# Kernel optimization log

Hardware: AMD Instinct MI355X
Metric: run time of the kernel (lower is better)

Reference implementation:

```python
import jax, jax.numpy as jnp
import numpy as np

B, T = 128, 512
V, P, K = 10002, 500, 20
DC, DP, DT = 300, 100, 50
D = DC + DP + DT
H = 256


def setup_inputs() -> dict:
    key = jax.random.key(0)
    ks = jax.random.split(key, 21)
    s = lambda i, shape: jax.random.normal(ks[i], shape, jnp.float32) * 0.05
    return dict(
        x=jax.random.randint(ks[0], (B, T), 0, V),
        y=jax.random.randint(ks[1], (B, T), 0, K),
        pre_tags=jax.random.randint(ks[2], (B, T), 0, K),
        pinyin_tags=jax.random.randint(ks[3], (B, T), 0, P),
        mask=jnp.ones((B, T), bool),
        char_emb=s(4, (V, DC)),
        tag_emb=s(5, (K, DT)),
        pinyin_emb=s(6, (P, DP)),
        w_ih_f=s(7, (4 * H, D)), w_hh_f=s(8, (4 * H, H)), b_ih_f=s(9, (4 * H,)), b_hh_f=s(10, (4 * H,)),
        w_ih_b=s(11, (4 * H, D)), w_hh_b=s(12, (4 * H, H)), b_ih_b=s(13, (4 * H,)), b_hh_b=s(14, (4 * H,)),
        w_out=s(15, (K, 2 * H)), b_out=s(16, (K,)),
        start_trans=s(17, (K,)), end_trans=s(18, (K,)), trans=s(19, (K, K)),
    )


def _lstm_dir(xs, w_ih, w_hh, b_ih, b_hh, reverse):
    # xs: [T,B,D]; precompute input projection for all steps (one big GEMM)
    pre = jnp.einsum('tbd,gd->tbg', xs, w_ih) + b_ih + b_hh  # [T,B,4H]
    bsz = xs.shape[1]

    def step(carry, gx):
        h, c = carry
        g = gx + h @ w_hh.T
        i, f, gg, o = jnp.split(g, 4, axis=-1)  # torch gate order i,f,g,o
        c = jax.nn.sigmoid(f) * c + jax.nn.sigmoid(i) * jnp.tanh(gg)
        h = jax.nn.sigmoid(o) * jnp.tanh(c)
        return (h, c), h

    init = (jnp.zeros((bsz, H), xs.dtype), jnp.zeros((bsz, H), xs.dtype))
    _, hs = jax.lax.scan(step, init, pre, reverse=reverse)
    return hs  # [T,B,H]


def _emissions(x, pre_tags, pinyin_tags, char_emb, tag_emb, pinyin_emb,
               w_ih_f, w_hh_f, b_ih_f, b_hh_f, w_ih_b, w_hh_b, b_ih_b, b_hh_b,
               w_out, b_out):
    emb = jnp.concatenate([char_emb[x], pinyin_emb[pinyin_tags], tag_emb[pre_tags]], axis=2)  # [B,T,D]
    xs = emb.transpose(1, 0, 2)  # [T,B,D]
    hf = _lstm_dir(xs, w_ih_f, w_hh_f, b_ih_f, b_hh_f, reverse=False)
    hb = _lstm_dir(xs, w_ih_b, w_hh_b, b_ih_b, b_hh_b, reverse=True)
    h = jnp.concatenate([hf, hb], axis=-1)  # [T,B,2H]
    return jnp.einsum('tbh,kh->tbk', h, w_out) + b_out  # emissions [T,B,K]


def _crf_nll(em, tags, mask, start, trans, end):
    # em [T,B,K] (time-major), torchcrf forward with reduction='sum'
    tg = tags.T  # [T,B]
    mk = mask.T.astype(em.dtype)  # [T,B]
    # gold-path score
    first = start[tg[0]] + jnp.take_along_axis(em[0], tg[0][:, None], 1)[:, 0]

    def num_step(score, inputs):
        e_t, t_prev, t_cur, m = inputs
        s = trans[t_prev, t_cur] + jnp.take_along_axis(e_t, t_cur[:, None], 1)[:, 0]
        return score + s * m, None

    score, _ = jax.lax.scan(num_step, first, (em[1:], tg[:-1], tg[1:], mk[1:]))
    last_idx = (mask.sum(1) - 1).astype(jnp.int32)
    last_tag = jnp.take_along_axis(tags, last_idx[:, None].astype(tags.dtype), 1)[:, 0]
    score = score + end[last_tag]
    # partition function via forward algorithm
    alpha0 = start[None, :] + em[0]  # [B,K]

    def den_step(alpha, inputs):
        e_t, m = inputs
        nxt = jax.nn.logsumexp(alpha[:, :, None] + trans[None, :, :] + e_t[:, None, :], axis=1)
        return jnp.where(m[:, None] > 0, nxt, alpha), None

    alpha, _ = jax.lax.scan(den_step, alpha0, (em[1:], mk[1:]))
    logZ = jax.nn.logsumexp(alpha + end[None, :], axis=1)
    llh = jnp.sum(score - logZ)
    return -llh  # module returns -crf(...)


def reference(x, y, pre_tags, pinyin_tags, mask, char_emb, tag_emb, pinyin_emb,
              w_ih_f, w_hh_f, b_ih_f, b_hh_f, w_ih_b, w_hh_b, b_ih_b, b_hh_b,
              w_out, b_out, start_trans, end_trans, trans):
    em = _emissions(x, pre_tags, pinyin_tags, char_emb, tag_emb, pinyin_emb,
                    w_ih_f, w_hh_f, b_ih_f, b_hh_f, w_ih_b, w_hh_b, b_ih_b, b_hh_b,
                    w_out, b_out)
    return _crf_nll(em, y, mask, start_trans, trans, end_trans)
```

## Files before the change

kernel.cpp:

```cpp
#include <hip/hip_runtime.h>
#include <hip/hip_bf16.h>

typedef __attribute__((ext_vector_type(8))) short short8;
typedef __attribute__((ext_vector_type(4))) float float4v;

#if __has_builtin(__builtin_amdgcn_sdot4)
#define DOT4(a, b, c) __builtin_amdgcn_sdot4((int)(a), (int)(b), (c), false)
#else
__device__ __forceinline__ int dot4_(int a, int b, int c) {
  c += (int)(signed char)(a) * (int)(signed char)(b);
  c += (int)(signed char)(a >> 8) * (int)(signed char)(b >> 8);
  c += (int)(signed char)(a >> 16) * (int)(signed char)(b >> 16);
  c += (a >> 24) * (b >> 24);
  return c;
}
#define DOT4(a, b, c) dot4_((int)(a), (int)(b), (c))
#endif

__device__ __forceinline__ float sigmoidf_(float x) {
  return __fdividef(1.f, 1.f + __expf(-x));
}
__device__ __forceinline__ float tanhf_(float x) {
  float e = __expf(2.f * x);
  return 1.f - __fdividef(2.f, e + 1.f);
}
__device__ __forceinline__ float bflo(unsigned int v) {
  return __uint_as_float(v << 16);
}
__device__ __forceinline__ float bfhi(unsigned int v) {
  return __uint_as_float(v & 0xffff0000u);
}

template <int CTRL>
__device__ __forceinline__ int qadd_i(int v) {
  return v + __builtin_amdgcn_update_dpp(0, v, CTRL, 0xF, 0xF, true);
}
template <int CTRL>
__device__ __forceinline__ float qmax_f(float v) {
  int r = __builtin_amdgcn_update_dpp(0, __float_as_int(v), CTRL, 0xF, 0xF, true);
  return fmaxf(v, __int_as_float(r));
}
#define XOR1 0xB1
#define XOR2 0x4E

__device__ __forceinline__ unsigned int pack4_(float4 v, float inv) {
  int b0 = (int)rintf(v.x * inv), b1 = (int)rintf(v.y * inv);
  int b2 = (int)rintf(v.z * inv), b3 = (int)rintf(v.w * inv);
  return (unsigned int)((b0 & 0xff) | ((b1 & 0xff) << 8) | ((b2 & 0xff) << 16) |
                        ((b3 & 0xff) << 24));
}

__global__ __launch_bounds__(256) void proj_gemm(
    const float* __restrict__ A, int rowsA, int Kdim, int col_off,
    const float* __restrict__ wf, const float* __restrict__ wb,
    const float* __restrict__ bf1, const float* __restrict__ bf2,
    const float* __restrict__ bb1, const float* __restrict__ bb2,
    __hip_bfloat16* __restrict__ out, int add_bias) {
  __shared__ __align__(16) __hip_bfloat16 As[64][40];
  __shared__ __align__(16) __hip_bfloat16 Bs[256][40];
  const int tid = threadIdx.x;
  const int m0 = blockIdx.x * 64, n0 = blockIdx.y * 256;
  const int lane = tid & 63, wave = tid >> 6;
  const int quad = lane >> 4, lm = lane & 15;
  float4v acc[16] = {};
  const int ksteps = (Kdim + 31) >> 5;
  const int r = tid >> 2, c0 = (tid & 3) << 3;
  const int rb = tid >> 4, cb = (tid & 15) * 2;
  for (int ks = 0; ks < ksteps; ++ks) {
    const int k0 = ks << 5;
#pragma unroll
    for (int e = 0; e < 8; ++e) {
      int kk = k0 + c0 + e;
      float av = (m0 + r < rowsA && kk < Kdim) ? A[(m0 + r) * Kdim + kk] : 0.f;
      As[r][c0 + e] = __float2bfloat16(av);
    }
#pragma unroll
    for (int j = 0; j < 16; ++j) {
      int n = n0 + rb + 16 * j;
      const float* __restrict__ wrow =
          (n < 1024) ? (wf + n * 450 + col_off) : (wb + (n - 1024) * 450 + col_off);
      int kk = k0 + cb;
      float b0 = 0.f, b1 = 0.f;
      if (kk < Kdim) {
        float2 v = *(const float2*)(wrow + kk);
        b0 = v.x;
        b1 = v.y;
      }
      Bs[rb + 16 * j][cb] = __float2bfloat16(b0);
      Bs[rb + 16 * j][cb + 1] = __float2bfloat16(b1);
    }
    __syncthreads();
    short8 af = *(const short8*)(&As[wave * 16 + lm][quad * 8]);
#pragma unroll
    for (int t = 0; t < 16; ++t) {
      short8 bf = *(const short8*)(&Bs[t * 16 + lm][quad * 8]);
      acc[t] = __builtin_amdgcn_mfma_f32_16x16x32_bf16(af, bf, acc[t], 0, 0, 0);
    }
    __syncthreads();
  }
#pragma unroll
  for (int t = 0; t < 16; ++t) {
#pragma unroll
    for (int rr = 0; rr < 4; ++rr) {
      int m = m0 + wave * 16 + quad * 4 + rr;
      int col = n0 + t * 16 + lm;
      if (m < rowsA) {
        float v = acc[t][rr];
        if (add_bias)
          v += (col < 1024) ? (bf1[col] + bf2[col]) : (bb1[col - 1024] + bb2[col - 1024]);
        int dir = col >> 10, r2 = col & 1023;
        int gate = r2 >> 8, u = r2 & 255;
        out[m * 2048 + dir * 1024 + u * 4 + gate] = __float2bfloat16(v);
      }
    }
  }
}

__global__ __launch_bounds__(256) void lstm_kernel(
    const float* __restrict__ whh_f, const float* __restrict__ whh_b,
    const int* __restrict__ x, const int* __restrict__ ptags, const int* __restrict__ gtags,
    const char* __restrict__ char_proj, const char* __restrict__ pin_proj,
    const char* __restrict__ tag_proj, __hip_bfloat16* __restrict__ h_out) {
  extern __shared__ __align__(16) char smem[];
  uint4* wlds = (uint4*)smem;
  int4* sidx = (int4*)(smem + 65536);
  signed char* hb = (signed char*)(smem + 73728);

  const int tid = threadIdx.x;
  const int q = tid >> 2, e = tid & 3;
  const int chain = blockIdx.x;
  const int dir = chain >> 7;
  const int b = chain & 127;
  const float* __restrict__ whh = dir ? whh_b : whh_f;

  sidx[tid] = make_int4(x[b * 512 + tid] * 4096, ptags[b * 512 + tid] * 4096,
                        gtags[b * 512 + tid] * 4096, 0);
  sidx[tid + 256] = make_int4(x[b * 512 + tid + 256] * 4096, ptags[b * 512 + tid + 256] * 4096,
                              gtags[b * 512 + tid + 256] * 4096, 0);
  if (tid < 32) ((int4*)hb)[tid] = make_int4(0, 0, 0, 0);

  unsigned int Wreg[12][16];
  float sc4[4];
#pragma unroll
  for (int rr = 0; rr < 16; ++rr) {
    const int unit = 4 * q + (rr >> 2), gate = rr & 3;
    const float* __restrict__ wr = whh + (gate * 256 + unit) * 256 + e * 64;
    float mx = 0.f;
#pragma unroll
    for (int k4 = 0; k4 < 16; ++k4) {
      float4 v = ((const float4*)wr)[k4];
      mx = fmaxf(mx, fmaxf(fmaxf(fabsf(v.x), fabsf(v.y)), fmaxf(fabsf(v.z), fabsf(v.w))));
    }
    mx = qmax_f<XOR1>(mx);
    mx = qmax_f<XOR2>(mx);
    float inv = (mx > 0.f) ? __fdividef(127.f, mx) : 0.f;
    float scv = (mx > 0.f) ? (mx / (127.f * 127.f)) : 0.f;
    if ((rr >> 2) == e) sc4[gate] = scv;
    if (rr < 12) {
#pragma unroll
      for (int k4 = 0; k4 < 16; ++k4) Wreg[rr][k4] = pack4_(((const float4*)wr)[k4], inv);
    } else {
      const int p = rr - 12;
#pragma unroll
      for (int c = 0; c < 4; ++c) {
        uint4 tv;
        tv.x = pack4_(((const float4*)wr)[c * 4 + 0], inv);
        tv.y = pack4_(((const float4*)wr)[c * 4 + 1], inv);
        tv.z = pack4_(((const float4*)wr)[c * 4 + 2], inv);
        tv.w = pack4_(((const float4*)wr)[c * 4 + 3], inv);
        wlds[(p * 4 + c) * 256 + tid] = tv;
      }
    }
  }
  __syncthreads();

  const int myu = tid;
  const int pre_off = dir * 2048 + myu * 8;
  float cst = 0.f;
  const uint4* wbase = wlds + tid;

  int t_cur = dir ? 511 : 0;
  uint2 pc, pp, pt;
  {
    int4 ix = sidx[t_cur];
    pc = *(const uint2*)(char_proj + ix.x + pre_off);
    pp = *(const uint2*)(pin_proj + ix.y + pre_off);
    pt = *(const uint2*)(tag_proj + ix.z + pre_off);
  }

  for (int s = 0; s < 512; ++s) {
    const int t = t_cur;
    const uint2 cv = pc, pv = pp, gv = pt;
    const int tn = dir ? (t > 0 ? t - 1 : 0) : (t < 511 ? t + 1 : 511);
    t_cur = tn;
    {
      int4 ix = sidx[tn];
      pc = *(const uint2*)(char_proj + ix.x + pre_off);
      pp = *(const uint2*)(pin_proj + ix.y + pre_off);
      pt = *(const uint2*)(tag_proj + ix.z + pre_off);
    }

    const signed char* hbase = hb + (s & 1) * 256 + e * 64;
    int acc[16] = {0, 0, 0, 0, 0, 0, 0, 0, 0, 0, 0, 0, 0, 0, 0, 0};
#pragma unroll
    for (int c = 0; c < 4; ++c) {
      uint4 H = *(const uint4*)(hbase + c * 16);
#pragma unroll
      for (int rr = 0; rr < 12; ++rr) {
        acc[rr] = DOT4(Wreg[rr][4 * c + 0], H.x, acc[rr]);
        acc[rr] = DOT4(Wreg[rr][4 * c + 1], H.y, acc[rr]);
        acc[rr] = DOT4(Wreg[rr][4 * c + 2], H.z, acc[rr]);
        acc[rr] = DOT4(Wreg[rr][4 * c + 3], H.w, acc[rr]);
      }
#pragma unroll
      for (int p = 0; p < 4; ++p) {
        uint4 wv = wbase[(p * 4 + c) * 256];
        acc[12 + p] = DOT4(wv.x, H.x, acc[12 + p]);
        acc[12 + p] = DOT4(wv.y, H.y, acc[12 + p]);
        acc[12 + p] = DOT4(wv.z, H.z, acc[12 + p]);
        acc[12 + p] = DOT4(wv.w, H.w, acc[12 + p]);
      }
    }
#pragma unroll
    for (int rr = 0; rr < 16; ++rr) {
      int v = qadd_i<XOR1>(acc[rr]);
      acc[rr] = qadd_i<XOR2>(v);
    }
    int ai = e == 0 ? acc[0] : (e == 1 ? acc[4] : (e == 2 ? acc[8] : acc[12]));
    int af = e == 0 ? acc[1] : (e == 1 ? acc[5] : (e == 2 ? acc[9] : acc[13]));
    int ag = e == 0 ? acc[2] : (e == 1 ? acc[6] : (e == 2 ? acc[10] : acc[14]));
    int ao = e == 0 ? acc[3] : (e == 1 ? acc[7] : (e == 2 ? acc[11] : acc[15]));
    float gi = bflo(cv.x) + bflo(pv.x) + bflo(gv.x) + (float)ai * sc4[0];
    float gf = bfhi(cv.x) + bfhi(pv.x) + bfhi(gv.x) + (float)af * sc4[1];
    float gg = bflo(cv.y) + bflo(pv.y) + bflo(gv.y) + (float)ag * sc4[2];
    float go = bfhi(cv.y) + bfhi(pv.y) + bfhi(gv.y) + (float)ao * sc4[3];
    cst = sigmoidf_(gf) * cst + sigmoidf_(gi) * tanhf_(gg);
    float hval = sigmoidf_(go) * tanhf_(cst);
    hb[((s + 1) & 1) * 256 + myu] = (signed char)(int)rintf(hval * 127.f);
    h_out[((size_t)chain * 512 + t) * 256 + myu] = __float2bfloat16(hval);
    __syncthreads();
  }
}

__global__ __launch_bounds__(256) void emis_kernel(
    const __hip_bfloat16* __restrict__ h_glob, const float* __restrict__ w_out,
    const float* __restrict__ b_out, float* __restrict__ em) {
  __shared__ __align__(16) __hip_bfloat16 As[64][40];
  __shared__ __align__(16) __hip_bfloat16 Bs[32][40];
  const int tid = threadIdx.x;
  const int n0 = blockIdx.x * 64;
  const int lane = tid & 63, wave = tid >> 6, quad = lane >> 4, lm = lane & 15;
  float4v acc[2] = {};
  const int r = tid >> 2, c0 = (tid & 3) << 3;
  const int rb = tid >> 3, cb = (tid & 7) << 2;
  for (int ks = 0; ks < 16; ++ks) {
    const int j0 = ks * 32;
    const int dirk = j0 >> 8, jin = j0 & 255;
    const int n = n0 + r, bb = n >> 9, tt = n & 511;
    const uint4* src =
        (const uint4*)(h_glob + ((size_t)(dirk * 128 + bb) * 512 + tt) * 256 + jin + c0);
    *(uint4*)(&As[r][c0]) = *src;
#pragma unroll
    for (int e = 0; e < 4; ++e) {
      float v = (rb < 20) ? w_out[rb * 512 + j0 + cb + e] : 0.f;
      Bs[rb][cb + e] = __float2bfloat16(v);
    }
    __syncthreads();
    short8 af = *(const short8*)(&As[wave * 16 + lm][quad * 8]);
#pragma unroll
    for (int t2 = 0; t2 < 2; ++t2) {
      short8 bf = *(const short8*)(&Bs[t2 * 16 + lm][quad * 8]);
      acc[t2] = __builtin_amdgcn_mfma_f32_16x16x32_bf16(af, bf, acc[t2], 0, 0, 0);
    }
    __syncthreads();
  }
#pragma unroll
  for (int t2 = 0; t2 < 2; ++t2) {
#pragma unroll
    for (int rr = 0; rr < 4; ++rr) {
      int col = t2 * 16 + lm;
      if (col < 20) {
        int n = n0 + wave * 16 + quad * 4 + rr;
        em[(size_t)n * 20 + col] = acc[t2][rr] + b_out[col];
      }
    }
  }
}

__global__ __launch_bounds__(64) void crf_kernel(
    const float* __restrict__ em, const int* __restrict__ y,
    const float* __restrict__ start_trans, const float* __restrict__ end_trans,
    const float* __restrict__ trans, float* __restrict__ partials) {
  const int b = blockIdx.x;
  const int lane = threadIdx.x;
  const int jj = lane < 20 ? lane : 19;
  const bool act = lane < 20;
  const float* __restrict__ emb = em + (size_t)b * 512 * 20;
  const int* __restrict__ yb = y + b * 512;

  float s_part = 0.f;
#pragma unroll
  for (int i = 0; i < 8; ++i) {
    int t = lane + 64 * i;
    int yc = yb[t];
    float v = emb[t * 20 + yc];
    v += (t == 0) ? start_trans[yc] : trans[yb[t - 1] * 20 + yc];
    s_part += v;
  }
#pragma unroll
  for (int k = 32; k >= 1; k >>= 1) s_part += __shfl_xor(s_part, k, 64);
  float score = s_part + end_trans[yb[511]];

  float ET[20];
#pragma unroll
  for (int i = 0; i < 20; ++i) ET[i] = __expf(trans[i * 20 + jj]);
  float alpha = act ? (start_trans[jj] + emb[jj]) : -1e30f;
  float P = alpha;
#pragma unroll
  for (int k = 32; k >= 1; k >>= 1) P = fmaxf(P, __shfl_xor(P, k, 64));

  float eC = emb[1 * 20 + jj];
  float eN = emb[2 * 20 + jj];
  for (int t = 1; t < 512; ++t) {
    if ((t & 15) == 0) {
      P = alpha;
#pragma unroll
      for (int k = 32; k >= 1; k >>= 1) P = fmaxf(P, __shfl_xor(P, k, 64));
    }
    float ex = __expf(alpha - P);
    float s0 = 0.f, s1 = 0.f;
#pragma unroll
    for (int i = 0; i < 20; i += 2) {
      float e0 = __int_as_float(__builtin_amdgcn_readlane(__float_as_int(ex), i));
      float e1 = __int_as_float(__builtin_amdgcn_readlane(__float_as_int(ex), i + 1));
      s0 = fmaf(e0, ET[i], s0);
      s1 = fmaf(e1, ET[i + 1], s1);
    }
    int tf = t + 2 < 512 ? t + 2 : 511;
    float eF = emb[tf * 20 + jj];
    if (act) alpha = P + __logf(s0 + s1) + eC;
    eC = eN;
    eN = eF;
  }
  float v = act ? (alpha + end_trans[jj]) : -1e30f;
  float Pz = v;
#pragma unroll
  for (int k = 32; k >= 1; k >>= 1) Pz = fmaxf(Pz, __shfl_xor(Pz, k, 64));
  float e2 = __expf(v - Pz);
#pragma unroll
  for (int k = 32; k >= 1; k >>= 1) e2 += __shfl_xor(e2, k, 64);
  float logZ = Pz + __logf(e2);
  if (lane == 0) partials[b] = logZ - score;
}

__global__ __launch_bounds__(128) void reduce_kernel(const float* __restrict__ partials,
                                                     float* __restrict__ out) {
  const int tid = threadIdx.x;
  float v = partials[tid];
#pragma unroll
  for (int k = 32; k >= 1; k >>= 1) v += __shfl_xor(v, k, 64);
  __shared__ float tmp[2];
  if ((tid & 63) == 0) tmp[tid >> 6] = v;
  __syncthreads();
  if (tid == 0) out[0] = tmp[0] + tmp[1];
}

extern "C" void kernel_launch(void* const* d_in, const int* in_sizes, int n_in,
                              void* d_out, int out_size, void* d_ws, size_t ws_size,
                              hipStream_t stream) {
  const int* x = (const int*)d_in[0];
  const int* y = (const int*)d_in[1];
  const int* pre_tags = (const int*)d_in[2];
  const int* pinyin_tags = (const int*)d_in[3];
  const float* char_emb = (const float*)d_in[5];
  const float* tag_emb = (const float*)d_in[6];
  const float* pinyin_emb = (const float*)d_in[7];
  const float* w_ih_f = (const float*)d_in[8];
  const float* w_hh_f = (const float*)d_in[9];
  const float* b_ih_f = (const float*)d_in[10];
  const float* b_hh_f = (const float*)d_in[11];
  const float* w_ih_b = (const float*)d_in[12];
  const float* w_hh_b = (const float*)d_in[13];
  const float* b_ih_b = (const float*)d_in[14];
  const float* b_hh_b = (const float*)d_in[15];
  const float* w_out = (const float*)d_in[16];
  const float* b_out = (const float*)d_in[17];
  const float* start_trans = (const float*)d_in[18];
  const float* end_trans = (const float*)d_in[19];
  const float* trans = (const float*)d_in[20];

  char* ws = (char*)d_ws;
  __hip_bfloat16* char_proj = (__hip_bfloat16*)(ws);
  __hip_bfloat16* pin_proj = (__hip_bfloat16*)(ws + 40968192);
  __hip_bfloat16* tag_proj = (__hip_bfloat16*)(ws + 43016192);
  __hip_bfloat16* h_glob = (__hip_bfloat16*)(ws + 43098112);
  float* em = (float*)(ws + 110206976);
  float* partials = (float*)(ws + 115449856);

  proj_gemm<<<dim3(157, 8), 256, 0, stream>>>(char_emb, 10002, 300, 0, w_ih_f, w_ih_b,
                                              nullptr, nullptr, nullptr, nullptr, char_proj, 0);
  proj_gemm<<<dim3(8, 8), 256, 0, stream>>>(pinyin_emb, 500, 100, 300, w_ih_f, w_ih_b,
                                            nullptr, nullptr, nullptr, nullptr, pin_proj, 0);
  proj_gemm<<<dim3(1, 8), 256, 0, stream>>>(tag_emb, 20, 50, 400, w_ih_f, w_ih_b,
                                            b_ih_f, b_hh_f, b_ih_b, b_hh_b, tag_proj, 1);

  const int lstm_lds = 74240;
  hipFuncSetAttribute((const void*)lstm_kernel, hipFuncAttributeMaxDynamicSharedMemorySize,
                      lstm_lds);
  lstm_kernel<<<256, 256, lstm_lds, stream>>>(w_hh_f, w_hh_b, x, pinyin_tags, pre_tags,
                                              (const char*)char_proj, (const char*)pin_proj,
                                              (const char*)tag_proj, h_glob);

  emis_kernel<<<1024, 256, 0, stream>>>(h_glob, w_out, b_out, em);
  crf_kernel<<<128, 64, 0, stream>>>(em, y, start_trans, end_trans, trans, partials);
  reduce_kernel<<<1, 128, 0, stream>>>(partials, (float*)d_out);
}
```

Before: 1.107 ms.

## Batch LSTM hidden-state writes via LDS history and enlarge projection GEMM tiles

The LSTM kernel now keeps the last 16 hidden states in an LDS history buffer and flushes them to global memory as coalesced 16-byte stores every 16 steps, instead of issuing one bf16 store per thread per step. The precomputed per-step index table in LDS is replaced by prefetching token indices from global memory two steps ahead. Separately, the projection GEMM tile grows from 64 to 128 rows with two MFMA accumulators per wave and float2 A loads. These changes target store traffic in the serial recurrence and weight reuse in the GEMM, at the cost of more LDS use, more accumulator registers, and global index loads inside the critical loop.

```diff
diff --git a/kernel.cpp b/kernel.cpp
--- a/kernel.cpp
+++ b/kernel.cpp
@@ -56,23 +56,29 @@
     const float* __restrict__ bf1, const float* __restrict__ bf2,
     const float* __restrict__ bb1, const float* __restrict__ bb2,
     __hip_bfloat16* __restrict__ out, int add_bias) {
-  __shared__ __align__(16) __hip_bfloat16 As[64][40];
+  __shared__ __align__(16) __hip_bfloat16 As[128][40];
   __shared__ __align__(16) __hip_bfloat16 Bs[256][40];
   const int tid = threadIdx.x;
-  const int m0 = blockIdx.x * 64, n0 = blockIdx.y * 256;
+  const int m0 = blockIdx.x * 128, n0 = blockIdx.y * 256;
   const int lane = tid & 63, wave = tid >> 6;
   const int quad = lane >> 4, lm = lane & 15;
-  float4v acc[16] = {};
+  float4v acc[2][16] = {};
   const int ksteps = (Kdim + 31) >> 5;
-  const int r = tid >> 2, c0 = (tid & 3) << 3;
+  const int r2 = tid >> 1, cbase = (tid & 1) << 4;
   const int rb = tid >> 4, cb = (tid & 15) * 2;
   for (int ks = 0; ks < ksteps; ++ks) {
     const int k0 = ks << 5;
 #pragma unroll
-    for (int e = 0; e < 8; ++e) {
-      int kk = k0 + c0 + e;
-      float av = (m0 + r < rowsA && kk < Kdim) ? A[(m0 + r) * Kdim + kk] : 0.f;
-      As[r][c0 + e] = __float2bfloat16(av);
+    for (int e2 = 0; e2 < 8; ++e2) {
+      int kk = k0 + cbase + 2 * e2;
+      float b0 = 0.f, b1 = 0.f;
+      if (m0 + r2 < rowsA && kk < Kdim) {
+        float2 v = *(const float2*)(A + (size_t)(m0 + r2) * Kdim + kk);
+        b0 = v.x;
+        b1 = v.y;
+      }
+      As[r2][cbase + 2 * e2] = __float2bfloat16(b0);
+      As[r2][cbase + 2 * e2 + 1] = __float2bfloat16(b1);
     }
 #pragma unroll
     for (int j = 0; j < 16; ++j) {
@@ -90,27 +96,32 @@
       Bs[rb + 16 * j][cb + 1] = __float2bfloat16(b1);
     }
     __syncthreads();
-    short8 af = *(const short8*)(&As[wave * 16 + lm][quad * 8]);
+    short8 af0 = *(const short8*)(&As[wave * 32 + lm][quad * 8]);
+    short8 af1 = *(const short8*)(&As[wave * 32 + 16 + lm][quad * 8]);
 #pragma unroll
     for (int t = 0; t < 16; ++t) {
       short8 bf = *(const short8*)(&Bs[t * 16 + lm][quad * 8]);
-      acc[t] = __builtin_amdgcn_mfma_f32_16x16x32_bf16(af, bf, acc[t], 0, 0, 0);
+      acc[0][t] = __builtin_amdgcn_mfma_f32_16x16x32_bf16(af0, bf, acc[0][t], 0, 0, 0);
+      acc[1][t] = __builtin_amdgcn_mfma_f32_16x16x32_bf16(af1, bf, acc[1][t], 0, 0, 0);
     }
     __syncthreads();
   }
 #pragma unroll
-  for (int t = 0; t < 16; ++t) {
-#pragma unroll
-    for (int rr = 0; rr < 4; ++rr) {
-      int m = m0 + wave * 16 + quad * 4 + rr;
-      int col = n0 + t * 16 + lm;
-      if (m < rowsA) {
-        float v = acc[t][rr];
-        if (add_bias)
-          v += (col < 1024) ? (bf1[col] + bf2[col]) : (bb1[col - 1024] + bb2[col - 1024]);
-        int dir = col >> 10, r2 = col & 1023;
-        int gate = r2 >> 8, u = r2 & 255;
-        out[m * 2048 + dir * 1024 + u * 4 + gate] = __float2bfloat16(v);
+  for (int mg = 0; mg < 2; ++mg) {
+#pragma unroll
+    for (int t = 0; t < 16; ++t) {
+#pragma unroll
+      for (int rr = 0; rr < 4; ++rr) {
+        int m = m0 + wave * 32 + mg * 16 + quad * 4 + rr;
+        int col = n0 + t * 16 + lm;
+        if (m < rowsA) {
+          float v = acc[mg][t][rr];
+          if (add_bias)
+            v += (col < 1024) ? (bf1[col] + bf2[col]) : (bb1[col - 1024] + bb2[col - 1024]);
+          int dir = col >> 10, rq = col & 1023;
+          int gate = rq >> 8, u = rq & 255;
+          out[m * 2048 + dir * 1024 + u * 4 + gate] = __float2bfloat16(v);
+        }
       }
     }
   }
@@ -123,8 +134,8 @@
     const char* __restrict__ tag_proj, __hip_bfloat16* __restrict__ h_out) {
   extern __shared__ __align__(16) char smem[];
   uint4* wlds = (uint4*)smem;
-  int4* sidx = (int4*)(smem + 65536);
-  signed char* hb = (signed char*)(smem + 73728);
+  __hip_bfloat16* hist = (__hip_bfloat16*)(smem + 65536);
+  signed char* hb = (signed char*)(smem + 81920);
 
   const int tid = threadIdx.x;
   const int q = tid >> 2, e = tid & 3;
@@ -132,11 +143,8 @@
   const int dir = chain >> 7;
   const int b = chain & 127;
   const float* __restrict__ whh = dir ? whh_b : whh_f;
-
-  sidx[tid] = make_int4(x[b * 512 + tid] * 4096, ptags[b * 512 + tid] * 4096,
-                        gtags[b * 512 + tid] * 4096, 0);
-  sidx[tid + 256] = make_int4(x[b * 512 + tid + 256] * 4096, ptags[b * 512 + tid + 256] * 4096,
-                              gtags[b * 512 + tid + 256] * 4096, 0);
+  const int boff = b * 512;
+
   if (tid < 32) ((int4*)hb)[tid] = make_int4(0, 0, 0, 0);
 
   unsigned int Wreg[12][16];
@@ -147,9 +155,12 @@
     const float* __restrict__ wr = whh + (gate * 256 + unit) * 256 + e * 64;
     float mx = 0.f;
 #pragma unroll
-    for (int k4 = 0; k4 < 16; ++k4) {
-      float4 v = ((const float4*)wr)[k4];
-      mx = fmaxf(mx, fmaxf(fmaxf(fabsf(v.x), fabsf(v.y)), fmaxf(fabsf(v.z), fabsf(v.w))));
+    for (int c4 = 0; c4 < 4; ++c4) {
+#pragma unroll
+      for (int j = 0; j < 4; ++j) {
+        float4 v = ((const float4*)wr)[c4 * 4 + j];
+        mx = fmaxf(mx, fmaxf(fmaxf(fabsf(v.x), fabsf(v.y)), fmaxf(fabsf(v.z), fabsf(v.w))));
+      }
     }
     mx = qmax_f<XOR1>(mx);
     mx = qmax_f<XOR2>(mx);
@@ -180,25 +191,23 @@
   const uint4* wbase = wlds + tid;
 
   int t_cur = dir ? 511 : 0;
-  uint2 pc, pp, pt;
-  {
-    int4 ix = sidx[t_cur];
-    pc = *(const uint2*)(char_proj + ix.x + pre_off);
-    pp = *(const uint2*)(pin_proj + ix.y + pre_off);
-    pt = *(const uint2*)(tag_proj + ix.z + pre_off);
-  }
+  int t_nxt = dir ? 510 : 1;
+  int xc = x[boff + t_cur], pc_i = ptags[boff + t_cur], gc_i = gtags[boff + t_cur];
+  uint2 vc = *(const uint2*)(char_proj + (size_t)xc * 4096 + pre_off);
+  uint2 vp = *(const uint2*)(pin_proj + (size_t)pc_i * 4096 + pre_off);
+  uint2 vg = *(const uint2*)(tag_proj + (size_t)gc_i * 4096 + pre_off);
+  int xn = x[boff + t_nxt], pn = ptags[boff + t_nxt], gn = gtags[boff + t_nxt];
 
   for (int s = 0; s < 512; ++s) {
     const int t = t_cur;
-    const uint2 cv = pc, pv = pp, gv = pt;
-    const int tn = dir ? (t > 0 ? t - 1 : 0) : (t < 511 ? t + 1 : 511);
-    t_cur = tn;
-    {
-      int4 ix = sidx[tn];
-      pc = *(const uint2*)(char_proj + ix.x + pre_off);
-      pp = *(const uint2*)(pin_proj + ix.y + pre_off);
-      pt = *(const uint2*)(tag_proj + ix.z + pre_off);
-    }
+    const uint2 cv = vc, pv = vp, gv = vg;
+    const int t_fut = dir ? (t_nxt > 0 ? t_nxt - 1 : 0) : (t_nxt < 511 ? t_nxt + 1 : 511);
+    vc = *(const uint2*)(char_proj + (size_t)xn * 4096 + pre_off);
+    vp = *(const uint2*)(pin_proj + (size_t)pn * 4096 + pre_off);
+    vg = *(const uint2*)(tag_proj + (size_t)gn * 4096 + pre_off);
+    xn = x[boff + t_fut];
+    pn = ptags[boff + t_fut];
+    gn = gtags[boff + t_fut];
 
     const signed char* hbase = hb + (s & 1) * 256 + e * 64;
     int acc[16] = {0, 0, 0, 0, 0, 0, 0, 0, 0, 0, 0, 0, 0, 0, 0, 0};
@@ -237,8 +246,24 @@
     cst = sigmoidf_(gf) * cst + sigmoidf_(gi) * tanhf_(gg);
     float hval = sigmoidf_(go) * tanhf_(cst);
     hb[((s + 1) & 1) * 256 + myu] = (signed char)(int)rintf(hval * 127.f);
-    h_out[((size_t)chain * 512 + t) * 256 + myu] = __float2bfloat16(hval);
+    hist[(s & 31) * 256 + myu] = __float2bfloat16(hval);
     __syncthreads();
+    if ((s & 15) == 15) {
+      const int slotBase = (s & 31) & ~15;
+      const int sBase = s - 15;
+#pragma unroll
+      for (int i = 0; i < 2; ++i) {
+        int c = i * 256 + tid;
+        int row = c >> 5;
+        int col16 = c & 31;
+        uint4 v = *(const uint4*)((const char*)hist + (slotBase + row) * 512 + col16 * 16);
+        int step_r = sBase + row;
+        int t_r = dir ? (511 - step_r) : step_r;
+        *(uint4*)((char*)h_out + ((size_t)(chain * 512 + t_r) * 256) * 2 + col16 * 16) = v;
+      }
+    }
+    t_cur = t_nxt;
+    t_nxt = t_fut;
   }
 }
 
@@ -397,14 +422,14 @@
   float* em = (float*)(ws + 110206976);
   float* partials = (float*)(ws + 115449856);
 
-  proj_gemm<<<dim3(157, 8), 256, 0, stream>>>(char_emb, 10002, 300, 0, w_ih_f, w_ih_b,
-                                              nullptr, nullptr, nullptr, nullptr, char_proj, 0);
-  proj_gemm<<<dim3(8, 8), 256, 0, stream>>>(pinyin_emb, 500, 100, 300, w_ih_f, w_ih_b,
+  proj_gemm<<<dim3(79, 8), 256, 0, stream>>>(char_emb, 10002, 300, 0, w_ih_f, w_ih_b,
+                                             nullptr, nullptr, nullptr, nullptr, char_proj, 0);
+  proj_gemm<<<dim3(4, 8), 256, 0, stream>>>(pinyin_emb, 500, 100, 300, w_ih_f, w_ih_b,
                                             nullptr, nullptr, nullptr, nullptr, pin_proj, 0);
   proj_gemm<<<dim3(1, 8), 256, 0, stream>>>(tag_emb, 20, 50, 400, w_ih_f, w_ih_b,
                                             b_ih_f, b_hh_f, b_ih_b, b_hh_b, tag_proj, 1);
 
-  const int lstm_lds = 74240;
+  const int lstm_lds = 82432;
   hipFuncSetAttribute((const void*)lstm_kernel, hipFuncAttributeMaxDynamicSharedMemorySize,
                       lstm_lds);
   lstm_kernel<<<256, 256, lstm_lds, stream>>>(w_hh_f, w_hh_b, x, pinyin_tags, pre_tags,
```

New measurement: 1.190 ms. 1.07x slower.
